# Kernel optimization log

Measured on AMD Instinct MI355X. Metric: run time of the kernel, lower is better.

Reference implementation:

```python
import jax, jax.numpy as jnp
import numpy as np

EMBED = 512
HEADS = 8
HEAD_DIM = EMBED // HEADS


def setup_inputs() -> dict:
    key = jax.random.key(0)
    ks = jax.random.split(key, 8)
    B, S = 2, 4096
    values = jax.random.normal(ks[0], (B, S, EMBED), dtype=jnp.float32)
    keys = jax.random.normal(ks[1], (B, S, EMBED), dtype=jnp.float32)
    query = jax.random.normal(ks[2], (B, S, EMBED), dtype=jnp.float32)
    # per-head projections (torch Linear: y = x @ W.T), head_dim x head_dim
    scale = 1.0 / np.sqrt(HEAD_DIM)
    Wv = jax.random.uniform(ks[3], (HEAD_DIM, HEAD_DIM), jnp.float32, -scale, scale)
    Wk = jax.random.uniform(ks[4], (HEAD_DIM, HEAD_DIM), jnp.float32, -scale, scale)
    Wq = jax.random.uniform(ks[5], (HEAD_DIM, HEAD_DIM), jnp.float32, -scale, scale)
    scale_o = 1.0 / np.sqrt(EMBED)
    Wo = jax.random.uniform(ks[6], (EMBED, EMBED), jnp.float32, -scale_o, scale_o)
    bo = jax.random.uniform(ks[7], (EMBED,), jnp.float32, -scale_o, scale_o)
    return {"values": values, "keys": keys, "query": query,
            "Wv": Wv, "Wk": Wk, "Wq": Wq, "Wo": Wo, "bo": bo}


def reference(values, keys, query, Wv, Wk, Wq, Wo, bo):
    N, S, _ = values.shape
    # split heads: [N, S, H, D]
    v = values.reshape(N, S, HEADS, HEAD_DIM)
    k = keys.reshape(N, S, HEADS, HEAD_DIM)
    q = query.reshape(N, S, HEADS, HEAD_DIM)
    # per-head linear projections (x @ W.T)
    v = jnp.einsum('nshd,ed->nshe', v, Wv)
    k = jnp.einsum('nshd,ed->nshe', k, Wk)
    q = jnp.einsum('nshd,ed->nshe', q, Wq)
    # energy: [N, H, Q, K]
    energy = jnp.einsum('nqhd,nkhd->nhqk', q, k)
    # NOTE: module scales by sqrt(embed_size), not sqrt(head_dim)
    attn = jax.nn.softmax(energy / jnp.sqrt(jnp.float32(EMBED)), axis=3)
    out = jnp.einsum('nhql,nlhd->nqhd', attn, v).reshape(N, S, EMBED)
    out = out @ Wo.T + bo
    return out
```

## Files before the change

### kernel.cpp

```cpp
#include <hip/hip_runtime.h>
#include <hip/hip_bf16.h>

#define S_LEN 4096
#define EMBED 512
#define HEADS 8
#define HD    64

typedef short v8s __attribute__((ext_vector_type(8)));
typedef float v4f __attribute__((ext_vector_type(4)));
typedef float v16f __attribute__((ext_vector_type(16)));
typedef unsigned int v4u __attribute__((ext_vector_type(4)));
typedef unsigned short u16;
typedef unsigned short v4us __attribute__((ext_vector_type(4)));

#define OFF_Q   0u
#define OFF_K   8388608u
#define OFF_VT  16777216u
#define OFF_AT  25165824u
#define OFF_WO  33554432u

static __device__ __forceinline__ short f2bf(float f) {
    __hip_bfloat16 h = __float2bfloat16(f);
    return __builtin_bit_cast(short, h);
}

static __device__ __forceinline__ v16f zero16() {
    v16f z;
#pragma unroll
    for (int i = 0; i < 16; ++i) z[i] = 0.f;
    return z;
}

static __device__ __forceinline__ unsigned cvtpk(float lo, float hi) {
    unsigned r;
    asm volatile("v_cvt_pk_bf16_f32 %0, %1, %2" : "=v"(r) : "v"(lo), "v"(hi));
    return r;
}

static __device__ __forceinline__ void pl32swap(unsigned &a, unsigned &b) {
    asm volatile("v_permlane32_swap_b32 %0, %1" : "+v"(a), "+v"(b));
}

static __device__ __forceinline__ void stage16(const void* g, void* l) {
    __builtin_amdgcn_global_load_lds(
        (const __attribute__((address_space(1))) unsigned int*)g,
        (__attribute__((address_space(3))) unsigned int*)l, 16, 0, 0);
}

__global__ __launch_bounds__(256) void proj_kernel(
    const float* __restrict__ xv, const float* __restrict__ xk,
    const float* __restrict__ xq,
    const float* __restrict__ Wv, const float* __restrict__ Wk,
    const float* __restrict__ Wq, const float* __restrict__ Wo,
    u16* __restrict__ q_bf, u16* __restrict__ k_bf,
    u16* __restrict__ vt_bf, u16* __restrict__ wo_bf)
{
    __shared__ u16 praw[24576];
    u16* const ldsX = praw;
    u16* const ldsW = praw + 12288;

    const int tid = threadIdx.x;
    const int lane = tid & 63;
    const int w = tid >> 6;
    const int lr = lane & 15;
    const int g  = lane >> 4;
    const int bid = blockIdx.x;
    const int bh = bid >> 6;
    const int stile = bid & 63;
    const int b = bh >> 3, h = bh & 7;
    const int s0 = stile * 64;

    {
        int idx = bid * 256 + tid;
        int n = idx >> 9, k = idx & 511;
        int dst = (((n >> 4) * 16 + (k >> 5)) * 64
                   + ((k >> 3) & 3) * 16 + (n & 15)) * 8 + (k & 7);
        wo_bf[dst] = (u16)f2bf(Wo[idx]);
    }

    {
        const float* xs[3] = { xq, xk, xv };
#pragma unroll
        for (int ti = 0; ti < 3; ++ti) {
            const float* src = xs[ti] + ((size_t)b*S_LEN + s0)*EMBED + h*HD;
            u16* dstT = ldsX + ti*4096;
#pragma unroll
            for (int p = 0; p < 4; ++p) {
                int c = tid + p*256;
                int row = c >> 4;
                int u   = (c & 15) >> 1;
                int su  = u ^ (row & 7);
                float4 f = *(const float4*)(src + (size_t)row*EMBED + (c & 15)*4);
                v4us pk;
                pk[0] = (u16)f2bf(f.x); pk[1] = (u16)f2bf(f.y);
                pk[2] = (u16)f2bf(f.z); pk[3] = (u16)f2bf(f.w);
                *(v4us*)(dstT + row*64 + su*8 + (c & 1)*4) = pk;
            }
        }
        const float* wsv[3] = { Wq, Wk, Wv };
#pragma unroll
        for (int ti = 0; ti < 3; ++ti) {
            u16* dstT = ldsW + ti*4096;
#pragma unroll
            for (int p = 0; p < 4; ++p) {
                int c = tid + p*256;
                int row = c >> 4;
                int u   = (c & 15) >> 1;
                int su  = u ^ (row & 7);
                float4 f = *(const float4*)(wsv[ti] + c*4);
                v4us pk;
                pk[0] = (u16)f2bf(f.x); pk[1] = (u16)f2bf(f.y);
                pk[2] = (u16)f2bf(f.z); pk[3] = (u16)f2bf(f.w);
                *(v4us*)(dstT + row*64 + su*8 + (c & 1)*4) = pk;
            }
        }
    }
    __syncthreads();

    const int rl = w*16 + lr;
    const int a8 = rl & 7;
    v8s aq0 = *(const v8s*)(ldsX        + rl*64 + ((g    ) ^ a8)*8);
    v8s aq1 = *(const v8s*)(ldsX        + rl*64 + ((4 + g) ^ a8)*8);
    v8s ak0 = *(const v8s*)(ldsX + 4096 + rl*64 + ((g    ) ^ a8)*8);
    v8s ak1 = *(const v8s*)(ldsX + 4096 + rl*64 + ((4 + g) ^ a8)*8);
    v8s av0 = *(const v8s*)(ldsX + 8192 + rl*64 + ((g    ) ^ a8)*8);
    v8s av1 = *(const v8s*)(ldsX + 8192 + rl*64 + ((4 + g) ^ a8)*8);
    __syncthreads();

    u16* const ldsQ = praw;
    u16* const ldsK = praw + 4096;
    u16* const ldsV = praw + 8192;

    const float qscale = 1.44269504088896f / 22.6274169979695f;
    const int w8 = lr & 7;

#pragma unroll
    for (int et = 0; et < 4; ++et) {
        v4f acc = (v4f){0.f,0.f,0.f,0.f};
        v8s b0 = *(const v8s*)(ldsW        + (et*16+lr)*64 + ((g    ) ^ w8)*8);
        v8s b1 = *(const v8s*)(ldsW        + (et*16+lr)*64 + ((4 + g) ^ w8)*8);
        acc = __builtin_amdgcn_mfma_f32_16x16x32_bf16(aq0, b0, acc, 0,0,0);
        acc = __builtin_amdgcn_mfma_f32_16x16x32_bf16(aq1, b1, acc, 0,0,0);
#pragma unroll
        for (int r = 0; r < 4; ++r) {
            int row = w*16 + g*4 + r;
            ldsQ[row*64 + et*16 + lr] = (u16)f2bf(acc[r]*qscale);
        }
    }
#pragma unroll
    for (int et = 0; et < 4; ++et) {
        v4f acc = (v4f){0.f,0.f,0.f,0.f};
        v8s b0 = *(const v8s*)(ldsW + 4096 + (et*16+lr)*64 + ((g    ) ^ w8)*8);
        v8s b1 = *(const v8s*)(ldsW + 4096 + (et*16+lr)*64 + ((4 + g) ^ w8)*8);
        acc = __builtin_amdgcn_mfma_f32_16x16x32_bf16(ak0, b0, acc, 0,0,0);
        acc = __builtin_amdgcn_mfma_f32_16x16x32_bf16(ak1, b1, acc, 0,0,0);
#pragma unroll
        for (int r = 0; r < 4; ++r) {
            int kvl = w*16 + g*4 + r;
            ldsK[(((kvl>>5)*4 + et)*64 + ((lr>>3)&1)*32 + (kvl&31))*8 + (lr&7)]
                = (u16)f2bf(acc[r]);
        }
    }
#pragma unroll
    for (int et = 0; et < 4; ++et) {
        v4f acc = (v4f){0.f,0.f,0.f,0.f};
        v8s a0 = *(const v8s*)(ldsW + 8192 + (et*16+lr)*64 + ((g    ) ^ w8)*8);
        v8s a1 = *(const v8s*)(ldsW + 8192 + (et*16+lr)*64 + ((4 + g) ^ w8)*8);
        acc = __builtin_amdgcn_mfma_f32_16x16x32_bf16(a0, av0, acc, 0,0,0);
        acc = __builtin_amdgcn_mfma_f32_16x16x32_bf16(a1, av1, acc, 0,0,0);
#pragma unroll
        for (int r = 0; r < 4; ++r) {
            int d   = et*16 + g*4 + r;
            int kvl = w*16 + lr;
            ldsV[(((d>>5)*4 + ((kvl>>4)&3))*64 + ((kvl>>3)&1)*32 + (d&31))*8 + (kvl&7)]
                = (u16)f2bf(acc[r]);
        }
    }
    __syncthreads();

    {
        const size_t qb = (size_t)bh * S_LEN * HD + (size_t)s0 * HD;
        const size_t kb = (size_t)(bh*128 + (s0>>5)) * 2048;
        const size_t vb = (size_t)(bh*64  + (s0>>6)) * 4096;
#pragma unroll
        for (int p = 0; p < 2; ++p) {
            int cid = tid + p*256;
            *(v8s*)(q_bf  + qb + (size_t)cid*8) = *(const v8s*)(ldsQ + cid*8);
            *(v8s*)(k_bf  + kb + (size_t)cid*8) = *(const v8s*)(ldsK + cid*8);
            *(v8s*)(vt_bf + vb + (size_t)cid*8) = *(const v8s*)(ldsV + cid*8);
        }
    }
}

__global__ __launch_bounds__(256, 4) void flash_kernel(
    const u16* __restrict__ q_bf, const u16* __restrict__ k_bf,
    const u16* __restrict__ vt_bf, u16* __restrict__ attn_buf)
{
    __shared__ char shraw[37888];

    const int tid = threadIdx.x;
    const int lane = tid & 63;
    const int w = tid >> 6;
    const int l31 = lane & 31;
    const int hi = lane >> 5;
    const int qsub = w >> 1;
    const int kvh  = w & 1;

    const int orig = blockIdx.x;
    const int wg = (orig & 7) * 128 + (orig >> 3);
    const int bh = wg >> 6;
    const int qt = wg & 63;
    const int s0 = qt * 64 + qsub * 32;

    const u16* __restrict__ Q = q_bf + (size_t)bh * S_LEN * HD;
    const char* __restrict__ KBp = (const char*)((const v8s*)k_bf  + (size_t)bh * 32768);
    const char* __restrict__ VBp = (const char*)((const v8s*)vt_bf + (size_t)bh * 32768);

    v8s qf[4];
#pragma unroll
    for (int dc = 0; dc < 4; ++dc)
        qf[dc] = *(const v8s*)(Q + (size_t)(s0 + l31)*HD + dc*16 + hi*8);

    v16f o0 = zero16(), o1 = zero16();
    float lsum = 0.f;

    v16f Zv = zero16();
    asm("" : "+v"(Zv));

    char* const myStage = shraw + kvh*8192 + qsub*4096;
    const int consK = kvh*8192;
    const int consV = kvh*8192 + 4096;
    const int t0 = kvh * 64;

#define STAGE(BUF, T32) do {                                                  \
    char* _l = myStage + (BUF)*16384;                                         \
    if (qsub == 0) {                                                          \
        const char* _g = KBp + (size_t)(T32)*4096 + lane*16;                  \
        stage16(_g,        _l);                                               \
        stage16(_g + 1024, _l + 1024);                                        \
        stage16(_g + 2048, _l + 2048);                                        \
        stage16(_g + 3072, _l + 3072);                                        \
    } else {                                                                  \
        const char* _g = VBp + (size_t)((T32)>>1)*8192 + ((T32)&1)*2048       \
                         + lane*16;                                           \
        stage16(_g,        _l);                                               \
        stage16(_g + 1024, _l + 1024);                                        \
        stage16(_g + 4096, _l + 2048);                                        \
        stage16(_g + 5120, _l + 3072);                                        \
    }                                                                         \
    __builtin_amdgcn_sched_barrier(0);   \
} while (0)

#define BODY(BUF) do {                                                        \
    const char* _bK = shraw + (BUF)*16384 + consK + lane*16;                  \
    const char* _bV = shraw + (BUF)*16384 + consV + lane*16;                  \
    v8s kf0 = *(const v8s*)(_bK);                                             \
    v8s kf1 = *(const v8s*)(_bK + 1024);                                      \
    v8s kf2 = *(const v8s*)(_bK + 2048);                                      \
    v8s kf3 = *(const v8s*)(_bK + 3072);                                      \
    v8s vf00 = *(const v8s*)(_bV);                                            \
    v8s vf01 = *(const v8s*)(_bV + 1024);                                     \
    v8s vf10 = *(const v8s*)(_bV + 2048);                                     \
    v8s vf11 = *(const v8s*)(_bV + 3072);                                     \
    __builtin_amdgcn_s_setprio(1);                                            \
    v16f s = __builtin_amdgcn_mfma_f32_32x32x16_bf16(kf0, qf[0], Zv, 0,0,0);  \
    s = __builtin_amdgcn_mfma_f32_32x32x16_bf16(kf1, qf[1], s, 0,0,0);        \
    s = __builtin_amdgcn_mfma_f32_32x32x16_bf16(kf2, qf[2], s, 0,0,0);        \
    s = __builtin_amdgcn_mfma_f32_32x32x16_bf16(kf3, qf[3], s, 0,0,0);        \
    __builtin_amdgcn_s_setprio(0);                                            \
    asm("" : "+v"(s));                                                        \
    float psA = 0.f, psB = 0.f;                                               \
    _Pragma("unroll")                                                         \
    for (int r = 0; r < 16; r += 2) {                                         \
        s[r]   = __builtin_amdgcn_exp2f(s[r]);   psA += s[r];                 \
        s[r+1] = __builtin_amdgcn_exp2f(s[r+1]); psB += s[r+1];               \
    }                                                                         \
    lsum += psA + psB;                                                        \
    v8s pa[2];                                                                \
    _Pragma("unroll")                                                         \
    for (int c = 0; c < 2; ++c) {                                             \
        const int rb = c * 8;                                                 \
        unsigned x0 = cvtpk(s[rb+0], s[rb+1]);                                \
        unsigned x1 = cvtpk(s[rb+2], s[rb+3]);                                \
        unsigned x2 = cvtpk(s[rb+4], s[rb+5]);                                \
        unsigned x3 = cvtpk(s[rb+6], s[rb+7]);                                \
        pl32swap(x0, x2);                                                     \
        pl32swap(x1, x3);                                                     \
        v4u u; u[0]=x0; u[1]=x1; u[2]=x2; u[3]=x3;                            \
        pa[c] = __builtin_bit_cast(v8s, u);                                   \
    }                                                                         \
    __builtin_amdgcn_s_setprio(1);                                            \
    o0 = __builtin_amdgcn_mfma_f32_32x32x16_bf16(vf00, pa[0], o0, 0,0,0);     \
    o0 = __builtin_amdgcn_mfma_f32_32x32x16_bf16(vf01, pa[1], o0, 0,0,0);     \
    o1 = __builtin_amdgcn_mfma_f32_32x32x16_bf16(vf10, pa[0], o1, 0,0,0);     \
    o1 = __builtin_amdgcn_mfma_f32_32x32x16_bf16(vf11, pa[1], o1, 0,0,0);     \
    __builtin_amdgcn_s_setprio(0);                                            \
} while (0)

    STAGE(0, t0);
    __syncthreads();
    for (int tt = 0; tt < 64; tt += 2) {
        STAGE(1, t0 + tt + 1);
        BODY(0);
        __syncthreads();
        if (tt != 62) STAGE(0, t0 + tt + 2);
        BODY(1);
        __syncthreads();
    }
#undef STAGE
#undef BODY

    float* fm = (float*)shraw;
    float* myp = fm + (w*64 + lane)*37;
#pragma unroll
    for (int c = 0; c < 4; ++c) {
        v4f t0v = (v4f){o0[c*4+0], o0[c*4+1], o0[c*4+2], o0[c*4+3]};
        v4f t1v = (v4f){o1[c*4+0], o1[c*4+1], o1[c*4+2], o1[c*4+3]};
        *(v4f*)(myp + c*4)      = t0v;
        *(v4f*)(myp + 16 + c*4) = t1v;
    }
    myp[32] = lsum;
    __syncthreads();

    const float L = fm[(w*64 + l31)*37 + 32] + fm[(w*64 + l31 + 32)*37 + 32]
                  + fm[((w^1)*64 + l31)*37 + 32] + fm[((w^1)*64 + l31 + 32)*37 + 32];
    const float inv = __builtin_amdgcn_rcpf(L);
    const float* pp = fm + ((w^1)*64 + lane)*37;

    const int b = bh >> 3, h = bh & 7;
    const int mt = (b * S_LEN + s0 + l31) >> 4;
    const int mr = l31 & 15;
    const size_t cb = ((size_t)mt * 16 + h*2 + kvh) * 64;
    if (kvh == 0) {
#pragma unroll
        for (int c = 0; c < 4; ++c) {
            v4us pk;
#pragma unroll
            for (int i = 0; i < 4; ++i)
                pk[i] = (u16)f2bf((o0[c*4+i] + pp[c*4+i]) * inv);
            *(v4us*)(attn_buf + (cb + c*16 + mr)*8 + hi*4) = pk;
        }
    } else {
#pragma unroll
        for (int c = 0; c < 4; ++c) {
            v4us pk;
#pragma unroll
            for (int i = 0; i < 4; ++i)
                pk[i] = (u16)f2bf((o1[c*4+i] + pp[16 + c*4+i]) * inv);
            *(v4us*)(attn_buf + (cb + c*16 + mr)*8 + hi*4) = pk;
        }
    }
}

__global__ __launch_bounds__(256) void oproj_kernel(
    const u16* __restrict__ attn_buf, const u16* __restrict__ wo_bf,
    const float* __restrict__ bo, float* __restrict__ out)
{
    const int tid = threadIdx.x;
    const int lane = tid & 63;
    const int w = tid >> 6;
    const int lr = lane & 15;
    const int g  = lane >> 4;
    const int bid = blockIdx.x;
    const int mt = (bid >> 3)*4 + w;
    const int m0 = mt * 16;
    const int n0 = (bid & 7)*64;
    const int ntb = (bid & 7)*4;

    const v8s* __restrict__ AF = (const v8s*)attn_buf;
    const v8s* __restrict__ WF = (const v8s*)wo_bf;

    v4f acc[4];
#pragma unroll
    for (int i = 0; i < 4; ++i) acc[i] = (v4f){0.f,0.f,0.f,0.f};

    for (int kk = 0; kk < EMBED/32; ++kk) {
        v8s af = AF[(size_t)(mt*16 + kk)*64 + lane];
#pragma unroll
        for (int nt = 0; nt < 4; ++nt) {
            v8s bf = WF[(size_t)((ntb + nt)*16 + kk)*64 + lane];
            acc[nt] = __builtin_amdgcn_mfma_f32_16x16x32_bf16(af, bf, acc[nt], 0,0,0);
        }
    }
#pragma unroll
    for (int nt = 0; nt < 4; ++nt) {
        float bias = bo[n0 + nt*16 + lr];
#pragma unroll
        for (int r = 0; r < 4; ++r) {
            out[(size_t)(m0 + g*4 + r)*EMBED + n0 + nt*16 + lr] = acc[nt][r] + bias;
        }
    }
}

extern "C" void kernel_launch(void* const* d_in, const int* in_sizes, int n_in,
                              void* d_out, int out_size, void* d_ws, size_t ws_size,
                              hipStream_t stream)
{
    const float* xv = (const float*)d_in[0];
    const float* xk = (const float*)d_in[1];
    const float* xq = (const float*)d_in[2];
    const float* Wv = (const float*)d_in[3];
    const float* Wk = (const float*)d_in[4];
    const float* Wq = (const float*)d_in[5];
    const float* Wo = (const float*)d_in[6];
    const float* bo = (const float*)d_in[7];

    char* ws = (char*)d_ws;
    u16* q_bf   = (u16*)(ws + OFF_Q);
    u16* k_bf   = (u16*)(ws + OFF_K);
    u16* vt_bf  = (u16*)(ws + OFF_VT);
    u16* at_buf = (u16*)(ws + OFF_AT);
    u16* wo_bf  = (u16*)(ws + OFF_WO);

    proj_kernel<<<1024, 256, 0, stream>>>(xv, xk, xq, Wv, Wk, Wq, Wo,
                                          q_bf, k_bf, vt_bf, wo_bf);
    flash_kernel<<<1024, 256, 0, stream>>>(q_bf, k_bf, vt_bf, at_buf);
    oproj_kernel<<<1024, 256, 0, stream>>>(at_buf, wo_bf, bo, (float*)d_out);
}
```

Measured before the change: 120.4 us.

## Process two query sub-tiles per wave to reuse staged K/V fragments

Each flash-attention workgroup now covers 128 query rows instead of 64, and each wave computes two 32-row query blocks against the same K and V fragments read from LDS. This halves the grid and the K/V global-to-LDS traffic per query row, and interleaves independent MFMA chains. In exchange it doubles the accumulator registers, lowers the occupancy target to 2 and enlarges the shared buffer used for the final cross-wave reduction. It also leaves fewer workgroups to spread across the compute units.

```diff
diff --git a/kernel.cpp b/kernel.cpp
--- a/kernel.cpp
+++ b/kernel.cpp
@@ -192,11 +192,11 @@
     }
 }
 
-__global__ __launch_bounds__(256, 4) void flash_kernel(
+__global__ __launch_bounds__(256, 2) void flash_kernel(
     const u16* __restrict__ q_bf, const u16* __restrict__ k_bf,
     const u16* __restrict__ vt_bf, u16* __restrict__ attn_buf)
 {
-    __shared__ char shraw[37888];
+    __shared__ char shraw[75776];
 
     const int tid = threadIdx.x;
     const int lane = tid & 63;
@@ -207,22 +207,26 @@
     const int kvh  = w & 1;
 
     const int orig = blockIdx.x;
-    const int wg = (orig & 7) * 128 + (orig >> 3);
-    const int bh = wg >> 6;
-    const int qt = wg & 63;
-    const int s0 = qt * 64 + qsub * 32;
+    const int wg = (orig & 7) * 64 + (orig >> 3);
+    const int bh = wg >> 5;
+    const int qt = wg & 31;
+    const int s0A = qt * 128 + qsub * 64;
+    const int s0B = s0A + 32;
 
     const u16* __restrict__ Q = q_bf + (size_t)bh * S_LEN * HD;
     const char* __restrict__ KBp = (const char*)((const v8s*)k_bf  + (size_t)bh * 32768);
     const char* __restrict__ VBp = (const char*)((const v8s*)vt_bf + (size_t)bh * 32768);
 
-    v8s qf[4];
-#pragma unroll
-    for (int dc = 0; dc < 4; ++dc)
-        qf[dc] = *(const v8s*)(Q + (size_t)(s0 + l31)*HD + dc*16 + hi*8);
-
-    v16f o0 = zero16(), o1 = zero16();
-    float lsum = 0.f;
+    v8s qa[4], qb[4];
+#pragma unroll
+    for (int dc = 0; dc < 4; ++dc) {
+        qa[dc] = *(const v8s*)(Q + (size_t)(s0A + l31)*HD + dc*16 + hi*8);
+        qb[dc] = *(const v8s*)(Q + (size_t)(s0B + l31)*HD + dc*16 + hi*8);
+    }
+
+    v16f o0A = zero16(), o1A = zero16();
+    v16f o0B = zero16(), o1B = zero16();
+    float lsA = 0.f, lsB = 0.f;
 
     v16f Zv = zero16();
     asm("" : "+v"(Zv));
@@ -263,37 +267,72 @@
     v8s vf10 = *(const v8s*)(_bV + 2048);                                     \
     v8s vf11 = *(const v8s*)(_bV + 3072);                                     \
     __builtin_amdgcn_s_setprio(1);                                            \
-    v16f s = __builtin_amdgcn_mfma_f32_32x32x16_bf16(kf0, qf[0], Zv, 0,0,0);  \
-    s = __builtin_amdgcn_mfma_f32_32x32x16_bf16(kf1, qf[1], s, 0,0,0);        \
-    s = __builtin_amdgcn_mfma_f32_32x32x16_bf16(kf2, qf[2], s, 0,0,0);        \
-    s = __builtin_amdgcn_mfma_f32_32x32x16_bf16(kf3, qf[3], s, 0,0,0);        \
+    v16f sA = __builtin_amdgcn_mfma_f32_32x32x16_bf16(kf0, qa[0], Zv, 0,0,0); \
+    v16f sB = __builtin_amdgcn_mfma_f32_32x32x16_bf16(kf0, qb[0], Zv, 0,0,0); \
+    sA = __builtin_amdgcn_mfma_f32_32x32x16_bf16(kf1, qa[1], sA, 0,0,0);      \
+    sB = __builtin_amdgcn_mfma_f32_32x32x16_bf16(kf1, qb[1], sB, 0,0,0);      \
+    sA = __builtin_amdgcn_mfma_f32_32x32x16_bf16(kf2, qa[2], sA, 0,0,0);      \
+    sB = __builtin_amdgcn_mfma_f32_32x32x16_bf16(kf2, qb[2], sB, 0,0,0);      \
+    sA = __builtin_amdgcn_mfma_f32_32x32x16_bf16(kf3, qa[3], sA, 0,0,0);      \
+    sB = __builtin_amdgcn_mfma_f32_32x32x16_bf16(kf3, qb[3], sB, 0,0,0);      \
     __builtin_amdgcn_s_setprio(0);                                            \
-    asm("" : "+v"(s));                                                        \
-    float psA = 0.f, psB = 0.f;                                               \
-    _Pragma("unroll")                                                         \
-    for (int r = 0; r < 16; r += 2) {                                         \
-        s[r]   = __builtin_amdgcn_exp2f(s[r]);   psA += s[r];                 \
-        s[r+1] = __builtin_amdgcn_exp2f(s[r+1]); psB += s[r+1];               \
+    asm("" : "+v"(sA));                                                       \
+    asm("" : "+v"(sB));                                                       \
+          \
+    {                                                                         \
+        float p0 = 0.f, p1 = 0.f;                                             \
+        _Pragma("unroll")                                                     \
+        for (int r = 0; r < 16; r += 2) {                                     \
+            sA[r]   = __builtin_amdgcn_exp2f(sA[r]);   p0 += sA[r];           \
+            sA[r+1] = __builtin_amdgcn_exp2f(sA[r+1]); p1 += sA[r+1];         \
+        }                                                                     \
+        lsA += p0 + p1;                                                       \
     }                                                                         \
-    lsum += psA + psB;                                                        \
-    v8s pa[2];                                                                \
-    _Pragma("unroll")                                                         \
-    for (int c = 0; c < 2; ++c) {                                             \
-        const int rb = c * 8;                                                 \
-        unsigned x0 = cvtpk(s[rb+0], s[rb+1]);                                \
-        unsigned x1 = cvtpk(s[rb+2], s[rb+3]);                                \
-        unsigned x2 = cvtpk(s[rb+4], s[rb+5]);                                \
-        unsigned x3 = cvtpk(s[rb+6], s[rb+7]);                                \
-        pl32swap(x0, x2);                                                     \
-        pl32swap(x1, x3);                                                     \
+    {                                                                         \
+        float p0 = 0.f, p1 = 0.f;                                             \
+        _Pragma("unroll")                                                     \
+        for (int r = 0; r < 16; r += 2) {                                     \
+            sB[r]   = __builtin_amdgcn_exp2f(sB[r]);   p0 += sB[r];           \
+            sB[r+1] = __builtin_amdgcn_exp2f(sB[r+1]); p1 += sB[r+1];         \
+        }                                                                     \
+        lsB += p0 + p1;                                                       \
+    }                                                                         \
+            \
+    v8s paA0, paA1, paB0, paB1;                                               \
+    {                                                                         \
+        unsigned x0 = cvtpk(sA[0], sA[1]), x1 = cvtpk(sA[2], sA[3]);          \
+        unsigned x2 = cvtpk(sA[4], sA[5]), x3 = cvtpk(sA[6], sA[7]);          \
+        pl32swap(x0, x2); pl32swap(x1, x3);                                   \
         v4u u; u[0]=x0; u[1]=x1; u[2]=x2; u[3]=x3;                            \
-        pa[c] = __builtin_bit_cast(v8s, u);                                   \
+        paA0 = __builtin_bit_cast(v8s, u);                                    \
+        unsigned y0 = cvtpk(sA[8], sA[9]),  y1 = cvtpk(sA[10], sA[11]);       \
+        unsigned y2 = cvtpk(sA[12], sA[13]), y3 = cvtpk(sA[14], sA[15]);      \
+        pl32swap(y0, y2); pl32swap(y1, y3);                                   \
+        v4u v; v[0]=y0; v[1]=y1; v[2]=y2; v[3]=y3;                            \
+        paA1 = __builtin_bit_cast(v8s, v);                                    \
     }                                                                         \
+    {                                                                         \
+        unsigned x0 = cvtpk(sB[0], sB[1]), x1 = cvtpk(sB[2], sB[3]);          \
+        unsigned x2 = cvtpk(sB[4], sB[5]), x3 = cvtpk(sB[6], sB[7]);          \
+        pl32swap(x0, x2); pl32swap(x1, x3);                                   \
+        v4u u; u[0]=x0; u[1]=x1; u[2]=x2; u[3]=x3;                            \
+        paB0 = __builtin_bit_cast(v8s, u);                                    \
+        unsigned y0 = cvtpk(sB[8], sB[9]),  y1 = cvtpk(sB[10], sB[11]);       \
+        unsigned y2 = cvtpk(sB[12], sB[13]), y3 = cvtpk(sB[14], sB[15]);      \
+        pl32swap(y0, y2); pl32swap(y1, y3);                                   \
+        v4u v; v[0]=y0; v[1]=y1; v[2]=y2; v[3]=y3;                            \
+        paB1 = __builtin_bit_cast(v8s, v);                                    \
+    }                                                                         \
+                                              \
     __builtin_amdgcn_s_setprio(1);                                            \
-    o0 = __builtin_amdgcn_mfma_f32_32x32x16_bf16(vf00, pa[0], o0, 0,0,0);     \
-    o0 = __builtin_amdgcn_mfma_f32_32x32x16_bf16(vf01, pa[1], o0, 0,0,0);     \
-    o1 = __builtin_amdgcn_mfma_f32_32x32x16_bf16(vf10, pa[0], o1, 0,0,0);     \
-    o1 = __builtin_amdgcn_mfma_f32_32x32x16_bf16(vf11, pa[1], o1, 0,0,0);     \
+    o0A = __builtin_amdgcn_mfma_f32_32x32x16_bf16(vf00, paA0, o0A, 0,0,0);    \
+    o0B = __builtin_amdgcn_mfma_f32_32x32x16_bf16(vf00, paB0, o0B, 0,0,0);    \
+    o0A = __builtin_amdgcn_mfma_f32_32x32x16_bf16(vf01, paA1, o0A, 0,0,0);    \
+    o0B = __builtin_amdgcn_mfma_f32_32x32x16_bf16(vf01, paB1, o0B, 0,0,0);    \
+    o1A = __builtin_amdgcn_mfma_f32_32x32x16_bf16(vf10, paA0, o1A, 0,0,0);    \
+    o1B = __builtin_amdgcn_mfma_f32_32x32x16_bf16(vf10, paB0, o1B, 0,0,0);    \
+    o1A = __builtin_amdgcn_mfma_f32_32x32x16_bf16(vf11, paA1, o1A, 0,0,0);    \
+    o1B = __builtin_amdgcn_mfma_f32_32x32x16_bf16(vf11, paB1, o1B, 0,0,0);    \
     __builtin_amdgcn_s_setprio(0);                                            \
 } while (0)
 
@@ -311,43 +350,52 @@
 #undef BODY
 
     float* fm = (float*)shraw;
-    float* myp = fm + (w*64 + lane)*37;
+    float* mypA = fm + ((w*2 + 0)*64 + lane)*37;
+    float* mypB = fm + ((w*2 + 1)*64 + lane)*37;
 #pragma unroll
     for (int c = 0; c < 4; ++c) {
-        v4f t0v = (v4f){o0[c*4+0], o0[c*4+1], o0[c*4+2], o0[c*4+3]};
-        v4f t1v = (v4f){o1[c*4+0], o1[c*4+1], o1[c*4+2], o1[c*4+3]};
-        *(v4f*)(myp + c*4)      = t0v;
-        *(v4f*)(myp + 16 + c*4) = t1v;
-    }
-    myp[32] = lsum;
+        *(v4f*)(mypA + c*4)      = (v4f){o0A[c*4+0], o0A[c*4+1], o0A[c*4+2], o0A[c*4+3]};
+        *(v4f*)(mypA + 16 + c*4) = (v4f){o1A[c*4+0], o1A[c*4+1], o1A[c*4+2], o1A[c*4+3]};
+        *(v4f*)(mypB + c*4)      = (v4f){o0B[c*4+0], o0B[c*4+1], o0B[c*4+2], o0B[c*4+3]};
+        *(v4f*)(mypB + 16 + c*4) = (v4f){o1B[c*4+0], o1B[c*4+1], o1B[c*4+2], o1B[c*4+3]};
+    }
+    mypA[32] = lsA;
+    mypB[32] = lsB;
     __syncthreads();
 
-    const float L = fm[(w*64 + l31)*37 + 32] + fm[(w*64 + l31 + 32)*37 + 32]
-                  + fm[((w^1)*64 + l31)*37 + 32] + fm[((w^1)*64 + l31 + 32)*37 + 32];
-    const float inv = __builtin_amdgcn_rcpf(L);
-    const float* pp = fm + ((w^1)*64 + lane)*37;
-
     const int b = bh >> 3, h = bh & 7;
-    const int mt = (b * S_LEN + s0 + l31) >> 4;
     const int mr = l31 & 15;
-    const size_t cb = ((size_t)mt * 16 + h*2 + kvh) * 64;
-    if (kvh == 0) {
-#pragma unroll
-        for (int c = 0; c < 4; ++c) {
-            v4us pk;
-#pragma unroll
-            for (int i = 0; i < 4; ++i)
-                pk[i] = (u16)f2bf((o0[c*4+i] + pp[c*4+i]) * inv);
-            *(v4us*)(attn_buf + (cb + c*16 + mr)*8 + hi*4) = pk;
-        }
-    } else {
-#pragma unroll
-        for (int c = 0; c < 4; ++c) {
-            v4us pk;
-#pragma unroll
-            for (int i = 0; i < 4; ++i)
-                pk[i] = (u16)f2bf((o1[c*4+i] + pp[16 + c*4+i]) * inv);
-            *(v4us*)(attn_buf + (cb + c*16 + mr)*8 + hi*4) = pk;
+#pragma unroll
+    for (int sub = 0; sub < 2; ++sub) {
+        const int own  = (w*2 + sub);
+        const int part = ((w^1)*2 + sub);
+        const float L = fm[(own*64  + l31)*37 + 32] + fm[(own*64  + l31 + 32)*37 + 32]
+                      + fm[(part*64 + l31)*37 + 32] + fm[(part*64 + l31 + 32)*37 + 32];
+        const float inv = __builtin_amdgcn_rcpf(L);
+        const float* pp = fm + (part*64 + lane)*37;
+        const float* oo = sub ? (const float*)&o0B : (const float*)&o0A;
+        const float* o1p = sub ? (const float*)&o1B : (const float*)&o1A;
+        const int s0 = sub ? s0B : s0A;
+        const int mt = (b * S_LEN + s0 + l31) >> 4;
+        const size_t cb = ((size_t)mt * 16 + h*2 + kvh) * 64;
+        if (kvh == 0) {
+#pragma unroll
+            for (int c = 0; c < 4; ++c) {
+                v4us pk;
+#pragma unroll
+                for (int i = 0; i < 4; ++i)
+                    pk[i] = (u16)f2bf((oo[c*4+i] + pp[c*4+i]) * inv);
+                *(v4us*)(attn_buf + (cb + c*16 + mr)*8 + hi*4) = pk;
+            }
+        } else {
+#pragma unroll
+            for (int c = 0; c < 4; ++c) {
+                v4us pk;
+#pragma unroll
+                for (int i = 0; i < 4; ++i)
+                    pk[i] = (u16)f2bf((o1p[c*4+i] + pp[16 + c*4+i]) * inv);
+                *(v4us*)(attn_buf + (cb + c*16 + mr)*8 + hi*4) = pk;
+            }
         }
     }
 }
@@ -414,6 +462,6 @@
 
     proj_kernel<<<1024, 256, 0, stream>>>(xv, xk, xq, Wv, Wk, Wq, Wo,
                                           q_bf, k_bf, vt_bf, wo_bf);
-    flash_kernel<<<1024, 256, 0, stream>>>(q_bf, k_bf, vt_bf, at_buf);
+    flash_kernel<<<512, 256, 0, stream>>>(q_bf, k_bf, vt_bf, at_buf);
     oproj_kernel<<<1024, 256, 0, stream>>>(at_buf, wo_bf, bo, (float*)d_out);
 }
```

Measured after the change: 111.2 us. 7.7% less time.
